# Performance work log

Measured on AMD Instinct MI355X. Metric: run time of the kernel, lower is better.

Reference implementation:

```python
import jax, jax.numpy as jnp
import numpy as np

B, XD, ZD, XE, H, NH = 8192, 4096, 1024, 64, 128, 4
NUM_STEPS, STEP, NOISE = 10, 0.01, 1.0
EPS = 1e-5


def setup_inputs() -> dict:
    key = jax.random.key(0)
    ks = jax.random.split(key, 16)
    w = lambda k, s: jax.random.normal(k, s, jnp.float32) * 0.02
    inp = {"x": jax.random.normal(ks[0], (B, XD), jnp.float32)}
    inp.update(
        px_W1=w(ks[1], (H, ZD)), px_b1=jnp.zeros(H, jnp.float32),
        px_W2=w(ks[2], (XD, H)), px_b2=jnp.zeros(XD, jnp.float32),
        emb_W=w(ks[3], (XE, XD)), emb_b=jnp.zeros(XE, jnp.float32),
        xp_W=w(ks[4], (H, XE)), xp_b=jnp.zeros(H, jnp.float32),
        zp_W=w(ks[5], (H, ZD)), zp_b=jnp.zeros(H, jnp.float32),
        sa_Wqkv=w(ks[6], (3 * H, H)), sa_bqkv=jnp.zeros(3 * H, jnp.float32),
        sa_Wo=w(ks[7], (H, H)), sa_bo=jnp.zeros(H, jnp.float32),
        ca_Wqkv=w(ks[8], (3 * H, H)), ca_bqkv=jnp.zeros(3 * H, jnp.float32),
        ca_Wo=w(ks[9], (H, H)), ca_bo=jnp.zeros(H, jnp.float32),
        ffn_W1=w(ks[10], (H, H)), ffn_b1=jnp.zeros(H, jnp.float32),
        ffn_W2=w(ks[11], (H, H)), ffn_b2=jnp.zeros(H, jnp.float32),
        ln1_g=jnp.ones(H, jnp.float32), ln1_b=jnp.zeros(H, jnp.float32),
        ln2_g=jnp.ones(H, jnp.float32), ln2_b=jnp.zeros(H, jnp.float32),
        ln3_g=jnp.ones(H, jnp.float32), ln3_b=jnp.zeros(H, jnp.float32),
        out_W=w(ks[12], (1, H)), out_b=jnp.zeros(1, jnp.float32),
    )
    return inp


def _ln(x, g, b):
    m = jnp.mean(x, -1, keepdims=True)
    v = jnp.var(x, -1, keepdims=True)
    return (x - m) * jax.lax.rsqrt(v + EPS) * g + b


def _mha(q, k, v, Wqkv, bqkv, Wo, bo):
    # torch nn.MultiheadAttention math, batch-first layout (B, S, E)
    E = q.shape[-1]
    d = E // NH
    Wq, Wk, Wv = jnp.split(Wqkv, 3, 0)
    bq, bk, bv = jnp.split(bqkv, 3, 0)
    hd = lambda t, W, bb: (t @ W.T + bb).reshape(t.shape[0], t.shape[1], NH, d)
    qh, kh, vh = hd(q, Wq, bq), hd(k, Wk, bk), hd(v, Wv, bv)
    s = jnp.einsum('bqhd,bkhd->bhqk', qh, kh) / jnp.sqrt(jnp.float32(d))
    a = jax.nn.softmax(s, -1)
    o = jnp.einsum('bhqk,bkhd->bqhd', a, vh).reshape(q.shape[0], q.shape[1], E)
    return o @ Wo.T + bo


def _forward(x, px_W1, px_b1, px_W2, px_b2, emb_W, emb_b, xp_W, xp_b, zp_W, zp_b,
             sa_Wqkv, sa_bqkv, sa_Wo, sa_bo, ca_Wqkv, ca_bqkv, ca_Wo, ca_bo,
             ffn_W1, ffn_b1, ffn_W2, ffn_b2, ln1_g, ln1_b, ln2_g, ln2_b,
             ln3_g, ln3_b, out_W, out_b):
    bsz = x.shape[0]
    px = lambda z: jax.nn.relu(z @ px_W1.T + px_b1) @ px_W2.T + px_b2
    grad_fn = jax.grad(lambda z: jnp.sum((px(z) - x) ** 2))
    ks = jax.random.split(jax.random.key(42), NUM_STEPS + 1)
    z0 = jax.random.normal(ks[0], (bsz, ZD), jnp.float32)

    def step(z, k):
        z = z - 0.5 * STEP * grad_fn(z)
        z = z + NOISE * jnp.sqrt(jnp.float32(STEP)) * jax.random.normal(k, z.shape, z.dtype)
        return z, None

    z, _ = jax.lax.scan(step, z0, ks[1:])
    z = jax.lax.stop_gradient(z)  # torch: z.detach()

    x_recon = px(z)                               # (B, XD)
    x_tok = (x @ emb_W.T + emb_b)[:, None, :]     # (B, 1, XE)
    z_lat = z[:, None, :]                         # (B, 1, ZD)
    x_h = x_tok @ xp_W.T + xp_b                   # (B, 1, H)
    z_h = z_lat @ zp_W.T + zp_b                   # (B, 1, H)
    sa = _mha(x_h, x_h, x_h, sa_Wqkv, sa_bqkv, sa_Wo, sa_bo)
    h1 = _ln(x_h + sa, ln1_g, ln1_b)
    ca = _mha(h1, z_h, z_h, ca_Wqkv, ca_bqkv, ca_Wo, ca_bo)
    h2 = _ln(h1 + ca, ln2_g, ln2_b)
    ff = jax.nn.relu(h2 @ ffn_W1.T + ffn_b1) @ ffn_W2.T + ffn_b2
    h3 = _ln(h2 + ff, ln3_g, ln3_b)
    y_pred = h3 @ out_W.T + out_b                 # (B, 1, 1)
    return x_recon, y_pred


def reference(x, px_W1, px_b1, px_W2, px_b2, emb_W, emb_b, xp_W, xp_b, zp_W, zp_b,
              sa_Wqkv, sa_bqkv, sa_Wo, sa_bo, ca_Wqkv, ca_bqkv, ca_Wo, ca_bo,
              ffn_W1, ffn_b1, ffn_W2, ffn_b2, ln1_g, ln1_b, ln2_g, ln2_b,
              ln3_g, ln3_b, out_W, out_b):
    return _forward(x, px_W1, px_b1, px_W2, px_b2, emb_W, emb_b, xp_W, xp_b,
                    zp_W, zp_b, sa_Wqkv, sa_bqkv, sa_Wo, sa_bo, ca_Wqkv,
                    ca_bqkv, ca_Wo, ca_bo, ffn_W1, ffn_b1, ffn_W2, ffn_b2,
                    ln1_g, ln1_b, ln2_g, ln2_b, ln3_g, ln3_b, out_W, out_b)
```

## Files before the change

### kernel.cpp

```cpp
#include <hip/hip_runtime.h>
#include <hip/hip_bf16.h>
#include <cstdint>
#include <cstddef>
#include <cmath>

#define B_     8192
#define XD_    4096
#define ZD_    1024
#define XE_    64
#define H_     128
#define ZN_    (B_*ZD_)

typedef __attribute__((ext_vector_type(8))) short short8_t;
typedef __attribute__((ext_vector_type(4))) float f32x4_t;
#define MFMA16(a,b,c) __builtin_amdgcn_mfma_f32_16x16x32_bf16((a),(b),(c),0,0,0)

__host__ __device__ __forceinline__ uint32_t rotl32_(uint32_t x, int r){
#ifdef __HIP_DEVICE_COMPILE__
  return __builtin_rotateleft32(x, (uint32_t)r);
#else
  return (x<<r)|(x>>(32-r));
#endif
}

__host__ __device__ __forceinline__ void tf2x32(uint32_t k0, uint32_t k1,
                                                uint32_t x0, uint32_t x1,
                                                uint32_t* o0, uint32_t* o1){
  uint32_t k2 = k0 ^ k1 ^ 0x1BD11BDAu;
  x0 += k0; x1 += k1;
  x0 += x1; x1 = rotl32_(x1,13); x1 ^= x0;
  x0 += x1; x1 = rotl32_(x1,15); x1 ^= x0;
  x0 += x1; x1 = rotl32_(x1,26); x1 ^= x0;
  x0 += x1; x1 = rotl32_(x1, 6); x1 ^= x0;
  x0 += k1; x1 += k2 + 1u;
  x0 += x1; x1 = rotl32_(x1,17); x1 ^= x0;
  x0 += x1; x1 = rotl32_(x1,29); x1 ^= x0;
  x0 += x1; x1 = rotl32_(x1,16); x1 ^= x0;
  x0 += x1; x1 = rotl32_(x1,24); x1 ^= x0;
  x0 += k2; x1 += k0 + 2u;
  x0 += x1; x1 = rotl32_(x1,13); x1 ^= x0;
  x0 += x1; x1 = rotl32_(x1,15); x1 ^= x0;
  x0 += x1; x1 = rotl32_(x1,26); x1 ^= x0;
  x0 += x1; x1 = rotl32_(x1, 6); x1 ^= x0;
  x0 += k0; x1 += k1 + 3u;
  x0 += x1; x1 = rotl32_(x1,17); x1 ^= x0;
  x0 += x1; x1 = rotl32_(x1,29); x1 ^= x0;
  x0 += x1; x1 = rotl32_(x1,16); x1 ^= x0;
  x0 += x1; x1 = rotl32_(x1,24); x1 ^= x0;
  x0 += k1; x1 += k2 + 4u;
  x0 += x1; x1 = rotl32_(x1,13); x1 ^= x0;
  x0 += x1; x1 = rotl32_(x1,15); x1 ^= x0;
  x0 += x1; x1 = rotl32_(x1,26); x1 ^= x0;
  x0 += x1; x1 = rotl32_(x1, 6); x1 ^= x0;
  x0 += k2; x1 += k0 + 5u;
  *o0 = x0; *o1 = x1;
}

__device__ __forceinline__ float erfinv_(float x){
  float w = -__logf(fmaf(-x, x, 1.0f));
  float p;
  if (w < 5.0f){
    w -= 2.5f;
    p = 2.81022636e-08f;
    p = fmaf(p, w, 3.43273939e-07f);
    p = fmaf(p, w, -3.5233877e-06f);
    p = fmaf(p, w, -4.39150654e-06f);
    p = fmaf(p, w, 0.00021858087f);
    p = fmaf(p, w, -0.00125372503f);
    p = fmaf(p, w, -0.00417768164f);
    p = fmaf(p, w, 0.246640727f);
    p = fmaf(p, w, 1.50140941f);
  } else {
    w = sqrtf(w) - 3.0f;
    p = -0.000200214257f;
    p = fmaf(p, w, 0.000100950558f);
    p = fmaf(p, w, 0.00134934322f);
    p = fmaf(p, w, -0.00367342844f);
    p = fmaf(p, w, 0.00573950773f);
    p = fmaf(p, w, -0.0076224613f);
    p = fmaf(p, w, 0.00943887047f);
    p = fmaf(p, w, 1.00167406f);
    p = fmaf(p, w, 2.83297682f);
  }
  return p * x;
}

__device__ __forceinline__ float bits_to_normal(uint32_t bits){
  float f = __uint_as_float((bits >> 9) | 0x3f800000u) - 1.0f;
  float u = fmaxf(-0.99999994f, fmaf(f, 2.0f, -0.99999994f));
  return 1.41421356f * erfinv_(u);
}

__device__ __forceinline__ float rng_normal(uint32_t k0, uint32_t k1, uint32_t idx){
  uint32_t o0, o1; tf2x32(k0, k1, 0u, idx, &o0, &o1);
  return bits_to_normal(o0 ^ o1);
}

__device__ __forceinline__ ushort f2bf(float f){
  return __builtin_bit_cast(ushort, __float2bfloat16(f));
}
__device__ __forceinline__ float bf2f(ushort u){ return __uint_as_float(((uint32_t)u) << 16); }

__device__ __forceinline__ void gen8(uint32_t k0, uint32_t k1, uint32_t base, uint4* g){
  union { ushort u[8]; uint4 q; } pk;
  #pragma unroll
  for (int j = 0; j < 8; ++j) pk.u[j] = f2bf(rng_normal(k0,k1,base+(uint32_t)j));
  *g = pk.q;
}

__global__ void k_prepAB(const float* __restrict__ saWo, const float* __restrict__ saWqkv,
                         const float* __restrict__ caWo, const float* __restrict__ caWqkv,
                         const float* __restrict__ sabqkv, const float* __restrict__ sabo,
                         const float* __restrict__ cabqkv, const float* __restrict__ cabo,
                         const float* __restrict__ W2, const float* __restrict__ pb2,
                         float* __restrict__ S, float* __restrict__ U,
                         float* __restrict__ s0, float* __restrict__ u0, float* __restrict__ cb,
                         uint32_t* __restrict__ dkeys){
  int blk = blockIdx.x, tid = threadIdx.x;
  if (blk < 512){
    int idx = (blk & 255) * 64 + tid;
    int i = idx >> 7, j = idx & 127;
    if (blk < 256){
      float acc = (i == j) ? 1.0f : 0.0f;
      for (int k = 0; k < H_; ++k) acc += saWo[i*H_ + k] * saWqkv[(2*H_ + k)*H_ + j];
      S[idx] = acc;
    } else {
      float acc = 0.0f;
      for (int k = 0; k < H_; ++k) acc += caWo[i*H_ + k] * caWqkv[(2*H_ + k)*H_ + j];
      U[idx] = acc;
    }
  } else {
    int b2 = blk - 512;
    if (b2 == 0 && tid == 0){
      for (uint32_t i = 0; i < 11; ++i){
        uint32_t a, b; tf2x32(0u, 42u, 0u, i, &a, &b);
        dkeys[2*i] = a; dkeys[2*i+1] = b;
      }
    }
    if (b2 < 2){
      int i = b2*64 + tid;
      float acc = sabo[i];
      for (int k = 0; k < H_; ++k) acc += saWo[i*H_ + k] * sabqkv[2*H_ + k];
      s0[i] = acc;
    } else if (b2 < 4){
      int i = (b2-2)*64 + tid;
      float acc = cabo[i];
      for (int k = 0; k < H_; ++k) acc += caWo[i*H_ + k] * cabqkv[2*H_ + k];
      u0[i] = acc;
    } else {
      int j = (b2-4)*64 + tid;
      float acc = 0.0f;
      for (int c = 0; c < XD_; ++c) acc += pb2[c] * W2[(size_t)c*H_ + j];
      cb[j] = acc;
    }
  }
}

__global__ void k_prepTR(const float* __restrict__ S, const float* __restrict__ U,
                         const float* __restrict__ xpW, const float* __restrict__ zpW,
                         const float* __restrict__ xpb, const float* __restrict__ zpb,
                         const float* __restrict__ s0, const float* __restrict__ u0,
                         float* __restrict__ T, float* __restrict__ R,
                         float* __restrict__ t0, float* __restrict__ r0v){
  int blk = blockIdx.x, tid = threadIdx.x;
  if (blk < 128){
    int idx = blk*64 + tid;
    int i = idx >> 6, e = idx & 63;
    float acc = 0.0f;
    for (int m = 0; m < H_; ++m) acc += S[i*H_ + m] * xpW[m*XE_ + e];
    T[idx] = acc;
  } else if (blk < 2176){
    int idx = (blk-128)*64 + tid;
    int i = idx >> 10, k = idx & 1023;
    float acc = 0.0f;
    for (int m = 0; m < H_; ++m) acc += U[i*H_ + m] * zpW[(size_t)m*ZD_ + k];
    R[idx] = acc;
  } else if (blk < 2178){
    int i = (blk-2176)*64 + tid;
    float acc = s0[i];
    for (int m = 0; m < H_; ++m) acc += S[i*H_ + m] * xpb[m];
    t0[i] = acc;
  } else {
    int i = (blk-2178)*64 + tid;
    float acc = u0[i];
    for (int m = 0; m < H_; ++m) acc += U[i*H_ + m] * zpb[m];
    r0v[i] = acc;
  }
}

__global__ void k_prepWM(const float* __restrict__ W2, const float* __restrict__ T,
                         const float* __restrict__ embW, const float* __restrict__ embb,
                         const float* __restrict__ t0, const float* __restrict__ W1,
                         const float* __restrict__ R,
                         ushort* __restrict__ WXT, float* __restrict__ q0,
                         float* __restrict__ Mpart, float* __restrict__ Gpart){
  if (blockIdx.x < 4096){
    int idx = blockIdx.x*256 + threadIdx.x;
    int j = idx >> 12, c = idx & 4095;
    float v;
    if (j < H_) v = W2[(size_t)c*H_ + j];
    else {
      int i = j - H_;
      float acc = 0.0f;
      for (int e = 0; e < XE_; ++e) acc += T[i*XE_ + e] * embW[(size_t)e*XD_ + c];
      v = acc;
    }
    WXT[idx] = f2bf(v);
    if (idx < H_){
      float acc = t0[idx];
      for (int e = 0; e < XE_; ++e) acc += T[idx*XE_ + e] * embb[e];
      q0[idx] = acc;
    }
  } else {
    int gid = (blockIdx.x - 4096)*256 + threadIdx.x;
    if (gid < 131072){
      int slice = gid >> 14, i = gid & 16383;
      int j1 = i >> 7, j2 = i & 127;
      int c0 = slice*512;
      float acc = 0.0f;
      for (int c = c0; c < c0+512; ++c)
        acc += W2[(size_t)c*H_ + j1] * W2[(size_t)c*H_ + j2];
      Mpart[(size_t)slice*16384 + i] = acc;
    } else {
      int g = gid - 131072;
      int slice = g >> 15, i2 = g & 32767;
      int i = i2 >> 7, k = i2 & 127;
      int m0 = slice*128;
      float acc = 0.0f;
      if (i < 128){
        for (int m = m0; m < m0+128; ++m)
          acc += W1[(size_t)i*ZD_ + m] * W1[(size_t)k*ZD_ + m];
      } else {
        for (int m = m0; m < m0+128; ++m)
          acc += W1[(size_t)k*ZD_ + m] * R[(size_t)(i-128)*ZD_ + m];
      }
      Gpart[(size_t)slice*32768 + i2] = acc;
    }
  }
}

__global__ void k_conv(const float* __restrict__ W2, const float* __restrict__ W1,
                       const float* __restrict__ R,
                       const float* __restrict__ Mpart, const float* __restrict__ Gpart,
                       ushort* __restrict__ W2bf, ushort* __restrict__ Mbf,
                       ushort* __restrict__ FBT, ushort* __restrict__ GGr){
  int idx = blockIdx.x*256 + threadIdx.x;
  if (idx < 524288) W2bf[idx] = f2bf(W2[idx]);
  else if (idx < 540672){
    int i = idx - 524288;
    float s = 0.0f;
    #pragma unroll
    for (int p = 0; p < 8; ++p) s += Mpart[(size_t)p*16384 + i];
    Mbf[i] = f2bf(2.0f*s);
  } else if (idx < 802816){
    int i = idx - 540672;
    int j    = i & 7;
    int lane = (i >> 3) & 63;
    int hh   = (i >> 9) & 1;
    int itt  = (i >> 10) & 15;
    int cf   = i >> 14;
    int srow = cf*16 + (lane & 15);
    int scol = itt*64 + hh*32 + ((lane >> 4) << 3) + j;
    float v = (srow < H_) ? W1[(size_t)srow*ZD_ + scol] : R[(size_t)(srow-H_)*ZD_ + scol];
    FBT[i] = f2bf(v);
  } else {
    int i = idx - 802816;
    float s = 0.0f;
    #pragma unroll
    for (int p = 0; p < 8; ++p) s += Gpart[(size_t)p*32768 + i];
    GGr[i] = f2bf(-0.005f*s);
  }
}

__global__ __launch_bounds__(256) void k_noiseproj(
    const ushort* __restrict__ FBT, const uint32_t* __restrict__ dkeys,
    float* __restrict__ y0c0, ushort* __restrict__ NWR){
  const int t = threadIdx.x, lane = t & 63, w = t >> 6;
  const int l15 = lane & 15, rq = (lane >> 4)*4, kq8 = (lane >> 4)*8;
  (void)kq8;
  const int gwid = blockIdx.x*4 + w;
  const int p = gwid >> 9, mb = gwid & 511;
  const int row0 = mb*16;
  const uint32_t k0 = dkeys[2*p], k1 = dkeys[2*p+1];
  const uint32_t rbase = (uint32_t)(row0 + l15)*1024u + (uint32_t)((lane >> 4)*8);
  f32x4_t acc[16] = {};
  #pragma unroll 1
  for (int it = 0; it < 16; ++it){
    uint4 br[16];
    {
      const ushort* fb = FBT + (size_t)(it*2)*512 + lane*8;
      #pragma unroll
      for (int cf = 0; cf < 16; ++cf) br[cf] = *(const uint4*)(fb + (size_t)cf*16384);
    }
    __builtin_amdgcn_sched_barrier(0);
    uint4 g0; gen8(k0, k1, rbase + (uint32_t)(it*64), &g0);
    short8_t a0 = __builtin_bit_cast(short8_t, g0);
    #pragma unroll
    for (int cf = 0; cf < 16; ++cf)
      acc[cf] = MFMA16(a0, __builtin_bit_cast(short8_t, br[cf]), acc[cf]);
    {
      const ushort* fb = FBT + (size_t)(it*2+1)*512 + lane*8;
      #pragma unroll
      for (int cf = 0; cf < 16; ++cf) br[cf] = *(const uint4*)(fb + (size_t)cf*16384);
    }
    __builtin_amdgcn_sched_barrier(0);
    uint4 g1; gen8(k0, k1, rbase + (uint32_t)(it*64 + 32), &g1);
    short8_t a1 = __builtin_bit_cast(short8_t, g1);
    #pragma unroll
    for (int cf = 0; cf < 16; ++cf)
      acc[cf] = MFMA16(a1, __builtin_bit_cast(short8_t, br[cf]), acc[cf]);
  }
  #pragma unroll
  for (int cf = 0; cf < 16; ++cf){
    int col = cf*16 + l15;
    #pragma unroll
    for (int r = 0; r < 4; ++r){
      int row = row0 + rq + r;
      float v = acc[cf][r];
      if (p == 0) y0c0[(size_t)row*256 + col] = v;
      else NWR[(size_t)(p-1)*2097152 + (size_t)row*256 + col] = f2bf(0.1f*v);
    }
  }
}

__global__ __launch_bounds__(256) void k_xpass_mfma(
    const float* __restrict__ x, const ushort* __restrict__ WXT,
    const float* __restrict__ cb, const float* __restrict__ q0,
    float* __restrict__ cneg, float* __restrict__ h1pre){
  __shared__ __align__(16) ushort xt[2][32*72];
  __shared__ __align__(16) ushort bt[2][128*72];
  const int t = threadIdx.x, lane = t & 63, w = t >> 6;
  const int bm = blockIdx.x >> 1, bn = blockIdx.x & 1;
  const int row0 = bm*32, ncol0 = bn*128;
  const int l15 = lane & 15, kq8 = (lane >> 4)*8, rq = (lane >> 4)*4;
  const int rt = w & 1, cb4 = (w >> 1)*4;
  const int xr = t >> 3, xk = (t & 7)*8;
  const int wn = t >> 1, wk = (t & 1)*32;
  f32x4_t acc[4] = {};
  {
    float4 v0 = *(const float4*)&x[(size_t)(row0+xr)*XD_ + xk];
    float4 v1 = *(const float4*)&x[(size_t)(row0+xr)*XD_ + xk + 4];
    union { ushort u[8]; uint4 q; } p;
    p.u[0]=f2bf(v0.x); p.u[1]=f2bf(v0.y); p.u[2]=f2bf(v0.z); p.u[3]=f2bf(v0.w);
    p.u[4]=f2bf(v1.x); p.u[5]=f2bf(v1.y); p.u[6]=f2bf(v1.z); p.u[7]=f2bf(v1.w);
    *(uint4*)&xt[0][xr*72 + xk] = p.q;
    const ushort* s = &WXT[(size_t)(ncol0+wn)*XD_ + wk];
    uint4 b0v=*(const uint4*)s, b1v=*(const uint4*)(s+8), b2v=*(const uint4*)(s+16), b3v=*(const uint4*)(s+24);
    ushort* d = &bt[0][wn*72 + wk];
    *(uint4*)d=b0v; *(uint4*)(d+8)=b1v; *(uint4*)(d+16)=b2v; *(uint4*)(d+24)=b3v;
  }
  float4 xv0, xv1; uint4 wb0, wb1, wb2, wb3;
  {
    xv0 = *(const float4*)&x[(size_t)(row0+xr)*XD_ + 64 + xk];
    xv1 = *(const float4*)&x[(size_t)(row0+xr)*XD_ + 64 + xk + 4];
    const ushort* s = &WXT[(size_t)(ncol0+wn)*XD_ + 64 + wk];
    wb0=*(const uint4*)s; wb1=*(const uint4*)(s+8); wb2=*(const uint4*)(s+16); wb3=*(const uint4*)(s+24);
  }
  #pragma unroll 1
  for (int it = 0; it < 64; ++it){
    __syncthreads();
    if (it < 63){
      union { ushort u[8]; uint4 q; } p;
      p.u[0]=f2bf(xv0.x); p.u[1]=f2bf(xv0.y); p.u[2]=f2bf(xv0.z); p.u[3]=f2bf(xv0.w);
      p.u[4]=f2bf(xv1.x); p.u[5]=f2bf(xv1.y); p.u[6]=f2bf(xv1.z); p.u[7]=f2bf(xv1.w);
      *(uint4*)&xt[(it+1)&1][xr*72 + xk] = p.q;
      ushort* d = &bt[(it+1)&1][wn*72 + wk];
      *(uint4*)d=wb0; *(uint4*)(d+8)=wb1; *(uint4*)(d+16)=wb2; *(uint4*)(d+24)=wb3;
    }
    if (it < 62){
      const int kt = (it+2)*64;
      xv0 = *(const float4*)&x[(size_t)(row0+xr)*XD_ + kt + xk];
      xv1 = *(const float4*)&x[(size_t)(row0+xr)*XD_ + kt + xk + 4];
      const ushort* s = &WXT[(size_t)(ncol0+wn)*XD_ + kt + wk];
      wb0=*(const uint4*)s; wb1=*(const uint4*)(s+8); wb2=*(const uint4*)(s+16); wb3=*(const uint4*)(s+24);
    }
    const ushort* xb = &xt[it&1][(rt*16+l15)*72];
    const ushort* bb = &bt[it&1][0];
    #pragma unroll
    for (int h = 0; h < 2; ++h){
      short8_t a = *(const short8_t*)(xb + h*32 + kq8);
      #pragma unroll
      for (int c = 0; c < 4; ++c){
        short8_t b = *(const short8_t*)(bb + ((cb4+c)*16+l15)*72 + h*32 + kq8);
        acc[c] = MFMA16(a, b, acc[c]);
      }
    }
  }
  #pragma unroll
  for (int c = 0; c < 4; ++c){
    int jl = (cb4+c)*16 + l15;
    #pragma unroll
    for (int r = 0; r < 4; ++r){
      int row = row0 + rt*16 + rq + r;
      float v = acc[c][r];
      if (bn == 0) cneg[(size_t)row*H_ + jl] = 2.0f*(cb[jl] - v);
      else         h1pre[(size_t)row*H_ + jl] = v + q0[jl];
    }
  }
}

__global__ __launch_bounds__(512) void k_lv2(
    const ushort* __restrict__ M2bf, const ushort* __restrict__ GGr,
    const float* __restrict__ y0c0, const ushort* __restrict__ NWR,
    const float* __restrict__ b1, const float* __restrict__ r0v,
    const float* __restrict__ cneg,
    ushort* __restrict__ hfin_bf, float* __restrict__ capre){
  __shared__ __align__(16) ushort abuf[16*136];
  __shared__ __align__(16) ushort glbuf[16*136];
  const int t = threadIdx.x, lane = t & 63, w = t >> 6;
  const int l15 = lane & 15, kq8 = (lane >> 4)*8, rq = (lane >> 4)*4;
  const int b0 = blockIdx.x * 16;
  const int myc = w*16 + l15;
  const int col2 = w*32 + l15;

  f32x4_t acc[2];
  #pragma unroll
  for (int nf = 0; nf < 2; ++nf)
    #pragma unroll
    for (int r = 0; r < 4; ++r)
      acc[nf][r] = y0c0[(size_t)(b0+rq+r)*256 + col2 + nf*16];
  float cn[4];
  #pragma unroll
  for (int r = 0; r < 4; ++r) cn[r] = cneg[(size_t)(b0+rq+r)*H_ + myc];
  float bb2[2];
  bb2[0] = (w < 4) ? b1[col2] : 0.0f;
  bb2[1] = (w < 4) ? b1[col2+16] : 0.0f;
  ushort nx[8];
  #pragma unroll
  for (int nf = 0; nf < 2; ++nf)
    #pragma unroll
    for (int r = 0; r < 4; ++r)
      nx[nf*4+r] = NWR[(size_t)(b0+rq+r)*256 + col2 + nf*16];

  #pragma unroll 1
  for (int s = 0; s < 10; ++s){
    if (w < 4){
      #pragma unroll
      for (int nf = 0; nf < 2; ++nf)
        #pragma unroll
        for (int r = 0; r < 4; ++r)
          abuf[(rq+r)*136 + col2 + nf*16] = f2bf(fmaxf(acc[nf][r] + bb2[nf], 0.0f));
    }
    __syncthreads();
    f32x4_t g2 = {};
    #pragma unroll
    for (int h = 0; h < 4; ++h){
      short8_t a = *(const short8_t*)&abuf[l15*136 + h*32 + kq8];
      short8_t b = *(const short8_t*)&M2bf[(size_t)myc*H_ + h*32 + kq8];
      g2 = MFMA16(a, b, g2);
    }
    #pragma unroll
    for (int r = 0; r < 4; ++r){
      float g = (abuf[(rq+r)*136 + myc] != 0) ? (g2[r] + cn[r]) : 0.0f;
      glbuf[(rq+r)*136 + myc] = f2bf(g);
    }
    __syncthreads();
    #pragma unroll
    for (int nf = 0; nf < 2; ++nf)
      #pragma unroll
      for (int h = 0; h < 4; ++h){
        short8_t a = *(const short8_t*)&glbuf[l15*136 + h*32 + kq8];
        short8_t b = *(const short8_t*)&GGr[(size_t)(col2 + nf*16)*H_ + h*32 + kq8];
        acc[nf] = MFMA16(a, b, acc[nf]);
      }
    #pragma unroll
    for (int nf = 0; nf < 2; ++nf)
      #pragma unroll
      for (int r = 0; r < 4; ++r)
        acc[nf][r] += bf2f(nx[nf*4+r]);
    if (s < 9){
      #pragma unroll
      for (int nf = 0; nf < 2; ++nf)
        #pragma unroll
        for (int r = 0; r < 4; ++r)
          nx[nf*4+r] = NWR[(size_t)(s+1)*2097152 + (size_t)(b0+rq+r)*256 + col2 + nf*16];
    }
    __syncthreads();
  }
  if (w < 4){
    #pragma unroll
    for (int nf = 0; nf < 2; ++nf)
      #pragma unroll
      for (int r = 0; r < 4; ++r)
        hfin_bf[(size_t)(b0+rq+r)*H_ + col2 + nf*16] = f2bf(fmaxf(acc[nf][r] + bb2[nf], 0.0f));
  } else {
    #pragma unroll
    for (int nf = 0; nf < 2; ++nf)
      #pragma unroll
      for (int r = 0; r < 4; ++r)
        capre[(size_t)(b0+rq+r)*H_ + (col2 + nf*16 - 128)] = acc[nf][r] + r0v[col2 + nf*16 - 128];
  }
}

__global__ __launch_bounds__(256) void k_xrecon_mfma(
    const ushort* __restrict__ hfin_bf, const ushort* __restrict__ W2bf,
    const float* __restrict__ b2, float* __restrict__ out){
  __shared__ __align__(16) ushort at[64*136];
  __shared__ __align__(16) ushort bt[128*136];
  const int tid = threadIdx.x, lane = tid & 63, w = tid >> 6;
  const int bm = blockIdx.x >> 5, bn = blockIdx.x & 31;
  const int row0 = bm*64, c0 = bn*128;
  const int l15 = lane & 15, kq8 = (lane >> 4)*8, rq = (lane >> 4)*4;
  { int r = tid >> 2, kq = (tid & 3)*32;
    const ushort* src = &hfin_bf[(size_t)(row0 + r)*H_ + kq];
    #pragma unroll
    for (int i = 0; i < 4; ++i) *(uint4*)&at[r*136 + kq + 8*i] = *(const uint4*)(src + 8*i);
  }
  { int n = tid >> 1, kh = (tid & 1)*64;
    const ushort* src = &W2bf[(size_t)(c0 + n)*H_ + kh];
    #pragma unroll
    for (int i = 0; i < 8; ++i) *(uint4*)&bt[n*136 + kh + 8*i] = *(const uint4*)(src + 8*i);
  }
  __syncthreads();
  f32x4_t acc[8] = {};
  #pragma unroll
  for (int k = 0; k < 4; ++k){
    short8_t a = *(const short8_t*)&at[(w*16 + l15)*136 + k*32 + kq8];
    #pragma unroll
    for (int nf = 0; nf < 8; ++nf){
      short8_t b = *(const short8_t*)&bt[(nf*16 + l15)*136 + k*32 + kq8];
      acc[nf] = MFMA16(a, b, acc[nf]);
    }
  }
  #pragma unroll
  for (int nf = 0; nf < 8; ++nf){
    int c = c0 + nf*16 + l15;
    float bbv = b2[c];
    #pragma unroll
    for (int r = 0; r < 4; ++r){
      int row = row0 + w*16 + rq + r;
      out[(size_t)row*XD_ + c] = acc[nf][r] + bbv;
    }
  }
}

__device__ __forceinline__ float wsum64(float v){
  #pragma unroll
  for (int off = 32; off > 0; off >>= 1) v += __shfl_xor(v, off, 64);
  return v;
}

__global__ __launch_bounds__(256) void k_tail(
    const float* __restrict__ h1pre, const float* __restrict__ capre,
    const float* __restrict__ ln1g, const float* __restrict__ ln1b,
    const float* __restrict__ ln2g, const float* __restrict__ ln2b,
    const float* __restrict__ ln3g, const float* __restrict__ ln3b,
    const float* __restrict__ fW1, const float* __restrict__ fb1,
    const float* __restrict__ fW2, const float* __restrict__ fb2,
    const float* __restrict__ outW, const float* __restrict__ outb,
    float* __restrict__ y){
  __shared__ float sh2[4][128];
  __shared__ float st1[4][128];
  const int tid = threadIdx.x;
  const int w = tid >> 6;
  const int l = tid & 63;
  const int b = blockIdx.x * 4 + w;
  const float* hp = h1pre + (size_t)b * H_;
  const float* cp = capre + (size_t)b * H_;
  float x0 = hp[l], x1 = hp[l+64];
  float m = wsum64(x0 + x1) * (1.0f/128.0f);
  float d0 = x0 - m, d1 = x1 - m;
  float v = wsum64(d0*d0 + d1*d1) * (1.0f/128.0f);
  float rs = rsqrtf(v + 1e-5f);
  float h1a = d0 * rs * ln1g[l]    + ln1b[l];
  float h1b = d1 * rs * ln1g[l+64] + ln1b[l+64];
  x0 = h1a + cp[l]; x1 = h1b + cp[l+64];
  m = wsum64(x0 + x1) * (1.0f/128.0f);
  d0 = x0 - m; d1 = x1 - m;
  v = wsum64(d0*d0 + d1*d1) * (1.0f/128.0f);
  rs = rsqrtf(v + 1e-5f);
  float h2a = d0 * rs * ln2g[l]    + ln2b[l];
  float h2b = d1 * rs * ln2g[l+64] + ln2b[l+64];
  sh2[w][l] = h2a; sh2[w][l+64] = h2b;
  __syncthreads();
  float ta = fb1[l], tb = fb1[l+64];
  #pragma unroll 8
  for (int m4 = 0; m4 < H_; m4 += 4){
    float4 hv = *(const float4*)&sh2[w][m4];
    float4 wa = *(const float4*)&fW1[(size_t)l*H_ + m4];
    float4 wb = *(const float4*)&fW1[(size_t)(l+64)*H_ + m4];
    ta = fmaf(wa.x, hv.x, ta); ta = fmaf(wa.y, hv.y, ta); ta = fmaf(wa.z, hv.z, ta); ta = fmaf(wa.w, hv.w, ta);
    tb = fmaf(wb.x, hv.x, tb); tb = fmaf(wb.y, hv.y, tb); tb = fmaf(wb.z, hv.z, tb); tb = fmaf(wb.w, hv.w, tb);
  }
  ta = fmaxf(ta, 0.0f); tb = fmaxf(tb, 0.0f);
  st1[w][l] = ta; st1[w][l+64] = tb;
  __syncthreads();
  float fa = fb2[l], fbv = fb2[l+64];
  #pragma unroll 8
  for (int m4 = 0; m4 < H_; m4 += 4){
    float4 tv = *(const float4*)&st1[w][m4];
    float4 wa = *(const float4*)&fW2[(size_t)l*H_ + m4];
    float4 wb = *(const float4*)&fW2[(size_t)(l+64)*H_ + m4];
    fa  = fmaf(wa.x, tv.x, fa);  fa  = fmaf(wa.y, tv.y, fa);  fa  = fmaf(wa.z, tv.z, fa);  fa  = fmaf(wa.w, tv.w, fa);
    fbv = fmaf(wb.x, tv.x, fbv); fbv = fmaf(wb.y, tv.y, fbv); fbv = fmaf(wb.z, tv.z, fbv); fbv = fmaf(wb.w, tv.w, fbv);
  }
  x0 = h2a + fa; x1 = h2b + fbv;
  m = wsum64(x0 + x1) * (1.0f/128.0f);
  d0 = x0 - m; d1 = x1 - m;
  v = wsum64(d0*d0 + d1*d1) * (1.0f/128.0f);
  rs = rsqrtf(v + 1e-5f);
  float h3a = d0 * rs * ln3g[l]    + ln3b[l];
  float h3b = d1 * rs * ln3g[l+64] + ln3b[l+64];
  float py = wsum64(outW[l]*h3a + outW[l+64]*h3b);
  if (l == 0) y[b] = py + outb[0];
}

extern "C" void kernel_launch(void* const* d_in, const int* in_sizes, int n_in,
                              void* d_out, int out_size, void* d_ws, size_t ws_size,
                              hipStream_t stream){
  const float* x      = (const float*)d_in[0];
  const float* pxW1   = (const float*)d_in[1];
  const float* pxb1   = (const float*)d_in[2];
  const float* pxW2   = (const float*)d_in[3];
  const float* pxb2   = (const float*)d_in[4];
  const float* embW   = (const float*)d_in[5];
  const float* embb   = (const float*)d_in[6];
  const float* xpW    = (const float*)d_in[7];
  const float* xpb    = (const float*)d_in[8];
  const float* zpW    = (const float*)d_in[9];
  const float* zpb    = (const float*)d_in[10];
  const float* saWqkv = (const float*)d_in[11];
  const float* sabqkv = (const float*)d_in[12];
  const float* saWo   = (const float*)d_in[13];
  const float* sabo   = (const float*)d_in[14];
  const float* caWqkv = (const float*)d_in[15];
  const float* cabqkv = (const float*)d_in[16];
  const float* caWo   = (const float*)d_in[17];
  const float* cabo   = (const float*)d_in[18];
  const float* fW1    = (const float*)d_in[19];
  const float* fb1    = (const float*)d_in[20];
  const float* fW2    = (const float*)d_in[21];
  const float* fb2    = (const float*)d_in[22];
  const float* ln1g   = (const float*)d_in[23];
  const float* ln1b   = (const float*)d_in[24];
  const float* ln2g   = (const float*)d_in[25];
  const float* ln2b   = (const float*)d_in[26];
  const float* ln3g   = (const float*)d_in[27];
  const float* ln3b   = (const float*)d_in[28];
  const float* outW   = (const float*)d_in[29];
  const float* outb   = (const float*)d_in[30];
  (void)in_sizes; (void)n_in; (void)out_size; (void)ws_size;

  float* ws    = (float*)d_ws;
  float* cneg  = ws;
  float* h1pre = cneg + (size_t)B_*H_;
  float* capre = h1pre + (size_t)B_*H_;
  float* Rm    = capre + (size_t)B_*H_;
  float* Sm    = Rm + (size_t)H_*ZD_;
  float* Um    = Sm + H_*H_;
  float* Tm    = Um + H_*H_;
  float* vs0   = Tm + H_*XE_;
  float* vu0   = vs0 + H_;
  float* vt0   = vu0 + H_;
  float* vq0   = vt0 + H_;
  float* vr0   = vq0 + H_;
  float* vcb   = vr0 + H_;
  float* Mpart = vcb + H_;
  float* Gpart = Mpart + 131072;
  uint32_t* dkeys = (uint32_t*)(Gpart + 262144);
  float* y0c0  = (float*)(dkeys + 32);
  ushort* WXT   = (ushort*)(y0c0 + (size_t)B_*256);
  ushort* W2bf  = WXT + (size_t)256*XD_;
  ushort* Mbf   = W2bf + (size_t)XD_*H_;
  ushort* FBT   = Mbf + H_*H_;
  ushort* GGr   = FBT + (size_t)256*ZD_;
  ushort* hfin  = GGr + (size_t)256*H_;
  ushort* NWR   = hfin + (size_t)B_*H_;

  float* xre   = (float*)d_out;
  float* ypred = xre + (size_t)B_*XD_;

  k_prepAB  <<<518,  64, 0, stream>>>(saWo, saWqkv, caWo, caWqkv, sabqkv, sabo,
                                      cabqkv, cabo, pxW2, pxb2, Sm, Um, vs0, vu0, vcb, dkeys);
  k_prepTR  <<<2180, 64, 0, stream>>>(Sm, Um, xpW, zpW, xpb, zpb, vs0, vu0, Tm, Rm, vt0, vr0);
  k_prepWM  <<<5632, 256, 0, stream>>>(pxW2, Tm, embW, embb, vt0, pxW1, Rm,
                                       WXT, vq0, Mpart, Gpart);
  k_conv    <<<3264, 256, 0, stream>>>(pxW2, pxW1, Rm, Mpart, Gpart, W2bf, Mbf, FBT, GGr);
  k_noiseproj <<<1408, 256, 0, stream>>>(FBT, dkeys, y0c0, NWR);
  k_xpass_mfma <<<512, 256, 0, stream>>>(x, WXT, vcb, vq0, cneg, h1pre);
  k_lv2     <<<512, 512, 0, stream>>>(Mbf, GGr, y0c0, NWR, pxb1, vr0, cneg, hfin, capre);
  k_xrecon_mfma <<<4096, 256, 0, stream>>>(hfin, W2bf, pxb2, xre);
  k_tail    <<<2048, 256, 0, stream>>>(h1pre, capre, ln1g, ln1b, ln2g, ln2b, ln3g, ln3b,
                                       fW1, fb1, fW2, fb2, outW, outb, ypred);
}
```

Measured before the change: 797.9 us.

## Merge noise projection with x-pass and fold tail into Langevin kernel

The noise-projection and x-pass GEMM kernels become one launch: blocks are interleaved 11:4 per group, so each group runs both kinds side by side and their work overlaps. The tail (layer norms, FFN, output head) now runs at the end of the Langevin kernel, reading cross-attention pre-activations from shared memory. This removes the capre global buffer and two launches. In exchange, the merged kernel carries the larger register and shared-memory footprint of both paths, which can lower occupancy, and the Langevin kernel gains serial tail work per block.

```diff
diff --git a/kernel.cpp b/kernel.cpp
--- a/kernel.cpp
+++ b/kernel.cpp
@@ -272,141 +272,159 @@
   }
 }
 
-__global__ __launch_bounds__(256) void k_noiseproj(
+__global__ __launch_bounds__(256) void k_npx2(
     const ushort* __restrict__ FBT, const uint32_t* __restrict__ dkeys,
-    float* __restrict__ y0c0, ushort* __restrict__ NWR){
+    float* __restrict__ y0c0, ushort* __restrict__ NWR,
+    const float* __restrict__ x, const ushort* __restrict__ WXT,
+    const float* __restrict__ cb, const float* __restrict__ q0v,
+    float* __restrict__ cneg, float* __restrict__ h1pre){
+  __shared__ __align__(16) ushort smem[23040];
   const int t = threadIdx.x, lane = t & 63, w = t >> 6;
   const int l15 = lane & 15, rq = (lane >> 4)*4, kq8 = (lane >> 4)*8;
-  (void)kq8;
-  const int gwid = blockIdx.x*4 + w;
-  const int p = gwid >> 9, mb = gwid & 511;
-  const int row0 = mb*16;
-  const uint32_t k0 = dkeys[2*p], k1 = dkeys[2*p+1];
-  const uint32_t rbase = (uint32_t)(row0 + l15)*1024u + (uint32_t)((lane >> 4)*8);
-  f32x4_t acc[16] = {};
-  #pragma unroll 1
-  for (int it = 0; it < 16; ++it){
-    uint4 br[16];
+  const int grp = blockIdx.x / 15, rem = blockIdx.x % 15;
+
+  if (rem < 11){
+    const int gwid = (grp*11 + rem)*4 + w;
+    const int p = gwid >> 9, mb = gwid & 511;
+    const int row0 = mb*16;
+    const uint32_t k0 = dkeys[2*p], k1 = dkeys[2*p+1];
+    const uint32_t rbase = (uint32_t)(row0 + l15)*1024u + (uint32_t)((lane >> 4)*8);
+    f32x4_t acc[16] = {};
+    #pragma unroll 1
+    for (int it = 0; it < 16; ++it){
+      uint4 br[16];
+      {
+        const ushort* fb = FBT + (size_t)(it*2)*512 + lane*8;
+        #pragma unroll
+        for (int cf = 0; cf < 16; ++cf) br[cf] = *(const uint4*)(fb + (size_t)cf*16384);
+      }
+      __builtin_amdgcn_sched_barrier(0);
+      uint4 g0; gen8(k0, k1, rbase + (uint32_t)(it*64), &g0);
+      short8_t a0 = __builtin_bit_cast(short8_t, g0);
+      #pragma unroll
+      for (int cf = 0; cf < 16; ++cf)
+        acc[cf] = MFMA16(a0, __builtin_bit_cast(short8_t, br[cf]), acc[cf]);
+      {
+        const ushort* fb = FBT + (size_t)(it*2+1)*512 + lane*8;
+        #pragma unroll
+        for (int cf = 0; cf < 16; ++cf) br[cf] = *(const uint4*)(fb + (size_t)cf*16384);
+      }
+      __builtin_amdgcn_sched_barrier(0);
+      uint4 g1; gen8(k0, k1, rbase + (uint32_t)(it*64 + 32), &g1);
+      short8_t a1 = __builtin_bit_cast(short8_t, g1);
+      #pragma unroll
+      for (int cf = 0; cf < 16; ++cf)
+        acc[cf] = MFMA16(a1, __builtin_bit_cast(short8_t, br[cf]), acc[cf]);
+    }
+    #pragma unroll
+    for (int cf = 0; cf < 16; ++cf){
+      int col = cf*16 + l15;
+      #pragma unroll
+      for (int r = 0; r < 4; ++r){
+        int row = row0 + rq + r;
+        float v = acc[cf][r];
+        if (p == 0) y0c0[(size_t)row*256 + col] = v;
+        else NWR[(size_t)(p-1)*2097152 + (size_t)row*256 + col] = f2bf(0.1f*v);
+      }
+    }
+  } else {
+    ushort* xt0 = smem;
+    ushort* xt1 = smem + 2304;
+    ushort* bt0 = smem + 4608;
+    ushort* bt1 = smem + 13824;
+    const int xp = grp*4 + (rem - 11);
+    const int bm = xp >> 1, bn = xp & 1;
+    const int row0 = bm*32, ncol0 = bn*128;
+    const int rt = w & 1, cb4 = (w >> 1)*4;
+    const int xr = t >> 3, xk = (t & 7)*8;
+    const int wn = t >> 1, wk = (t & 1)*32;
+    f32x4_t acc[4] = {};
     {
-      const ushort* fb = FBT + (size_t)(it*2)*512 + lane*8;
-      #pragma unroll
-      for (int cf = 0; cf < 16; ++cf) br[cf] = *(const uint4*)(fb + (size_t)cf*16384);
-    }
-    __builtin_amdgcn_sched_barrier(0);
-    uint4 g0; gen8(k0, k1, rbase + (uint32_t)(it*64), &g0);
-    short8_t a0 = __builtin_bit_cast(short8_t, g0);
-    #pragma unroll
-    for (int cf = 0; cf < 16; ++cf)
-      acc[cf] = MFMA16(a0, __builtin_bit_cast(short8_t, br[cf]), acc[cf]);
+      float4 v0 = *(const float4*)&x[(size_t)(row0+xr)*XD_ + xk];
+      float4 v1 = *(const float4*)&x[(size_t)(row0+xr)*XD_ + xk + 4];
+      union { ushort u[8]; uint4 q; } p;
+      p.u[0]=f2bf(v0.x); p.u[1]=f2bf(v0.y); p.u[2]=f2bf(v0.z); p.u[3]=f2bf(v0.w);
+      p.u[4]=f2bf(v1.x); p.u[5]=f2bf(v1.y); p.u[6]=f2bf(v1.z); p.u[7]=f2bf(v1.w);
+      *(uint4*)&xt0[xr*72 + xk] = p.q;
+      const ushort* s = &WXT[(size_t)(ncol0+wn)*XD_ + wk];
+      uint4 b0v=*(const uint4*)s, b1v=*(const uint4*)(s+8), b2v=*(const uint4*)(s+16), b3v=*(const uint4*)(s+24);
+      ushort* d = &bt0[wn*72 + wk];
+      *(uint4*)d=b0v; *(uint4*)(d+8)=b1v; *(uint4*)(d+16)=b2v; *(uint4*)(d+24)=b3v;
+    }
+    float4 xv0, xv1; uint4 wb0, wb1, wb2, wb3;
     {
-      const ushort* fb = FBT + (size_t)(it*2+1)*512 + lane*8;
-      #pragma unroll
-      for (int cf = 0; cf < 16; ++cf) br[cf] = *(const uint4*)(fb + (size_t)cf*16384);
-    }
-    __builtin_amdgcn_sched_barrier(0);
-    uint4 g1; gen8(k0, k1, rbase + (uint32_t)(it*64 + 32), &g1);
-    short8_t a1 = __builtin_bit_cast(short8_t, g1);
-    #pragma unroll
-    for (int cf = 0; cf < 16; ++cf)
-      acc[cf] = MFMA16(a1, __builtin_bit_cast(short8_t, br[cf]), acc[cf]);
-  }
+      xv0 = *(const float4*)&x[(size_t)(row0+xr)*XD_ + 64 + xk];
+      xv1 = *(const float4*)&x[(size_t)(row0+xr)*XD_ + 64 + xk + 4];
+      const ushort* s = &WXT[(size_t)(ncol0+wn)*XD_ + 64 + wk];
+      wb0=*(const uint4*)s; wb1=*(const uint4*)(s+8); wb2=*(const uint4*)(s+16); wb3=*(const uint4*)(s+24);
+    }
+    #pragma unroll 1
+    for (int it = 0; it < 64; ++it){
+      __syncthreads();
+      if (it < 63){
+        union { ushort u[8]; uint4 q; } p;
+        p.u[0]=f2bf(xv0.x); p.u[1]=f2bf(xv0.y); p.u[2]=f2bf(xv0.z); p.u[3]=f2bf(xv0.w);
+        p.u[4]=f2bf(xv1.x); p.u[5]=f2bf(xv1.y); p.u[6]=f2bf(xv1.z); p.u[7]=f2bf(xv1.w);
+        *(uint4*)&(((it+1)&1) ? xt1 : xt0)[xr*72 + xk] = p.q;
+        ushort* d = &(((it+1)&1) ? bt1 : bt0)[wn*72 + wk];
+        *(uint4*)d=wb0; *(uint4*)(d+8)=wb1; *(uint4*)(d+16)=wb2; *(uint4*)(d+24)=wb3;
+      }
+      if (it < 62){
+        const int kt = (it+2)*64;
+        xv0 = *(const float4*)&x[(size_t)(row0+xr)*XD_ + kt + xk];
+        xv1 = *(const float4*)&x[(size_t)(row0+xr)*XD_ + kt + xk + 4];
+        const ushort* s = &WXT[(size_t)(ncol0+wn)*XD_ + kt + wk];
+        wb0=*(const uint4*)s; wb1=*(const uint4*)(s+8); wb2=*(const uint4*)(s+16); wb3=*(const uint4*)(s+24);
+      }
+      const ushort* xb = &((it&1) ? xt1 : xt0)[(rt*16+l15)*72];
+      const ushort* bb = (it&1) ? bt1 : bt0;
+      #pragma unroll
+      for (int h = 0; h < 2; ++h){
+        short8_t a = *(const short8_t*)(xb + h*32 + kq8);
+        #pragma unroll
+        for (int c = 0; c < 4; ++c){
+          short8_t b = *(const short8_t*)(bb + ((cb4+c)*16+l15)*72 + h*32 + kq8);
+          acc[c] = MFMA16(a, b, acc[c]);
+        }
+      }
+    }
+    #pragma unroll
+    for (int c = 0; c < 4; ++c){
+      int jl = (cb4+c)*16 + l15;
+      #pragma unroll
+      for (int r = 0; r < 4; ++r){
+        int row = row0 + rt*16 + rq + r;
+        float v = acc[c][r];
+        if (bn == 0) cneg[(size_t)row*H_ + jl] = 2.0f*(cb[jl] - v);
+        else         h1pre[(size_t)row*H_ + jl] = v + q0v[jl];
+      }
+    }
+  }
+}
+
+__device__ __forceinline__ float wsum64(float v){
   #pragma unroll
-  for (int cf = 0; cf < 16; ++cf){
-    int col = cf*16 + l15;
-    #pragma unroll
-    for (int r = 0; r < 4; ++r){
-      int row = row0 + rq + r;
-      float v = acc[cf][r];
-      if (p == 0) y0c0[(size_t)row*256 + col] = v;
-      else NWR[(size_t)(p-1)*2097152 + (size_t)row*256 + col] = f2bf(0.1f*v);
-    }
-  }
-}
-
-__global__ __launch_bounds__(256) void k_xpass_mfma(
-    const float* __restrict__ x, const ushort* __restrict__ WXT,
-    const float* __restrict__ cb, const float* __restrict__ q0,
-    float* __restrict__ cneg, float* __restrict__ h1pre){
-  __shared__ __align__(16) ushort xt[2][32*72];
-  __shared__ __align__(16) ushort bt[2][128*72];
-  const int t = threadIdx.x, lane = t & 63, w = t >> 6;
-  const int bm = blockIdx.x >> 1, bn = blockIdx.x & 1;
-  const int row0 = bm*32, ncol0 = bn*128;
-  const int l15 = lane & 15, kq8 = (lane >> 4)*8, rq = (lane >> 4)*4;
-  const int rt = w & 1, cb4 = (w >> 1)*4;
-  const int xr = t >> 3, xk = (t & 7)*8;
-  const int wn = t >> 1, wk = (t & 1)*32;
-  f32x4_t acc[4] = {};
-  {
-    float4 v0 = *(const float4*)&x[(size_t)(row0+xr)*XD_ + xk];
-    float4 v1 = *(const float4*)&x[(size_t)(row0+xr)*XD_ + xk + 4];
-    union { ushort u[8]; uint4 q; } p;
-    p.u[0]=f2bf(v0.x); p.u[1]=f2bf(v0.y); p.u[2]=f2bf(v0.z); p.u[3]=f2bf(v0.w);
-    p.u[4]=f2bf(v1.x); p.u[5]=f2bf(v1.y); p.u[6]=f2bf(v1.z); p.u[7]=f2bf(v1.w);
-    *(uint4*)&xt[0][xr*72 + xk] = p.q;
-    const ushort* s = &WXT[(size_t)(ncol0+wn)*XD_ + wk];
-    uint4 b0v=*(const uint4*)s, b1v=*(const uint4*)(s+8), b2v=*(const uint4*)(s+16), b3v=*(const uint4*)(s+24);
-    ushort* d = &bt[0][wn*72 + wk];
-    *(uint4*)d=b0v; *(uint4*)(d+8)=b1v; *(uint4*)(d+16)=b2v; *(uint4*)(d+24)=b3v;
-  }
-  float4 xv0, xv1; uint4 wb0, wb1, wb2, wb3;
-  {
-    xv0 = *(const float4*)&x[(size_t)(row0+xr)*XD_ + 64 + xk];
-    xv1 = *(const float4*)&x[(size_t)(row0+xr)*XD_ + 64 + xk + 4];
-    const ushort* s = &WXT[(size_t)(ncol0+wn)*XD_ + 64 + wk];
-    wb0=*(const uint4*)s; wb1=*(const uint4*)(s+8); wb2=*(const uint4*)(s+16); wb3=*(const uint4*)(s+24);
-  }
-  #pragma unroll 1
-  for (int it = 0; it < 64; ++it){
-    __syncthreads();
-    if (it < 63){
-      union { ushort u[8]; uint4 q; } p;
-      p.u[0]=f2bf(xv0.x); p.u[1]=f2bf(xv0.y); p.u[2]=f2bf(xv0.z); p.u[3]=f2bf(xv0.w);
-      p.u[4]=f2bf(xv1.x); p.u[5]=f2bf(xv1.y); p.u[6]=f2bf(xv1.z); p.u[7]=f2bf(xv1.w);
-      *(uint4*)&xt[(it+1)&1][xr*72 + xk] = p.q;
-      ushort* d = &bt[(it+1)&1][wn*72 + wk];
-      *(uint4*)d=wb0; *(uint4*)(d+8)=wb1; *(uint4*)(d+16)=wb2; *(uint4*)(d+24)=wb3;
-    }
-    if (it < 62){
-      const int kt = (it+2)*64;
-      xv0 = *(const float4*)&x[(size_t)(row0+xr)*XD_ + kt + xk];
-      xv1 = *(const float4*)&x[(size_t)(row0+xr)*XD_ + kt + xk + 4];
-      const ushort* s = &WXT[(size_t)(ncol0+wn)*XD_ + kt + wk];
-      wb0=*(const uint4*)s; wb1=*(const uint4*)(s+8); wb2=*(const uint4*)(s+16); wb3=*(const uint4*)(s+24);
-    }
-    const ushort* xb = &xt[it&1][(rt*16+l15)*72];
-    const ushort* bb = &bt[it&1][0];
-    #pragma unroll
-    for (int h = 0; h < 2; ++h){
-      short8_t a = *(const short8_t*)(xb + h*32 + kq8);
-      #pragma unroll
-      for (int c = 0; c < 4; ++c){
-        short8_t b = *(const short8_t*)(bb + ((cb4+c)*16+l15)*72 + h*32 + kq8);
-        acc[c] = MFMA16(a, b, acc[c]);
-      }
-    }
-  }
-  #pragma unroll
-  for (int c = 0; c < 4; ++c){
-    int jl = (cb4+c)*16 + l15;
-    #pragma unroll
-    for (int r = 0; r < 4; ++r){
-      int row = row0 + rt*16 + rq + r;
-      float v = acc[c][r];
-      if (bn == 0) cneg[(size_t)row*H_ + jl] = 2.0f*(cb[jl] - v);
-      else         h1pre[(size_t)row*H_ + jl] = v + q0[jl];
-    }
-  }
-}
-
-__global__ __launch_bounds__(512) void k_lv2(
+  for (int off = 32; off > 0; off >>= 1) v += __shfl_xor(v, off, 64);
+  return v;
+}
+
+__global__ __launch_bounds__(512) void k_lv2t(
     const ushort* __restrict__ M2bf, const ushort* __restrict__ GGr,
     const float* __restrict__ y0c0, const ushort* __restrict__ NWR,
     const float* __restrict__ b1, const float* __restrict__ r0v,
-    const float* __restrict__ cneg,
-    ushort* __restrict__ hfin_bf, float* __restrict__ capre){
+    const float* __restrict__ cneg, const float* __restrict__ h1pre,
+    const float* __restrict__ ln1g, const float* __restrict__ ln1b,
+    const float* __restrict__ ln2g, const float* __restrict__ ln2b,
+    const float* __restrict__ ln3g, const float* __restrict__ ln3b,
+    const float* __restrict__ fW1, const float* __restrict__ fb1,
+    const float* __restrict__ fW2, const float* __restrict__ fb2,
+    const float* __restrict__ outW, const float* __restrict__ outb,
+    ushort* __restrict__ hfin_bf, float* __restrict__ ypred){
   __shared__ __align__(16) ushort abuf[16*136];
   __shared__ __align__(16) ushort glbuf[16*136];
+  __shared__ __align__(16) float caplds[16][132];
+  __shared__ __align__(16) float rowA[8][132];
+  __shared__ __align__(16) float rowB[8][132];
   const int t = threadIdx.x, lane = t & 63, w = t >> 6;
   const int l15 = lane & 15, kq8 = (lane >> 4)*8, rq = (lane >> 4)*4;
   const int b0 = blockIdx.x * 16;
@@ -488,7 +506,60 @@
     for (int nf = 0; nf < 2; ++nf)
       #pragma unroll
       for (int r = 0; r < 4; ++r)
-        capre[(size_t)(b0+rq+r)*H_ + (col2 + nf*16 - 128)] = acc[nf][r] + r0v[col2 + nf*16 - 128];
+        caplds[rq+r][col2 + nf*16 - 128] = acc[nf][r] + r0v[col2 + nf*16 - 128];
+  }
+  __syncthreads();
+
+  const int l = lane;
+  #pragma unroll 1
+  for (int j = 0; j < 2; ++j){
+    const int rloc = w*2 + j;
+    const int rr = b0 + rloc;
+    const float* hp = h1pre + (size_t)rr * H_;
+    float x0 = hp[l], x1 = hp[l+64];
+    float m = wsum64(x0 + x1) * (1.0f/128.0f);
+    float d0 = x0 - m, d1 = x1 - m;
+    float v = wsum64(d0*d0 + d1*d1) * (1.0f/128.0f);
+    float rs = rsqrtf(v + 1e-5f);
+    float h1a = d0 * rs * ln1g[l]    + ln1b[l];
+    float h1b = d1 * rs * ln1g[l+64] + ln1b[l+64];
+    x0 = h1a + caplds[rloc][l]; x1 = h1b + caplds[rloc][l+64];
+    m = wsum64(x0 + x1) * (1.0f/128.0f);
+    d0 = x0 - m; d1 = x1 - m;
+    v = wsum64(d0*d0 + d1*d1) * (1.0f/128.0f);
+    rs = rsqrtf(v + 1e-5f);
+    float h2a = d0 * rs * ln2g[l]    + ln2b[l];
+    float h2b = d1 * rs * ln2g[l+64] + ln2b[l+64];
+    rowA[w][l] = h2a; rowA[w][l+64] = h2b;
+    float ta = fb1[l], tb = fb1[l+64];
+    #pragma unroll 8
+    for (int m4 = 0; m4 < H_; m4 += 4){
+      float4 hv = *(const float4*)&rowA[w][m4];
+      float4 wa = *(const float4*)&fW1[(size_t)l*H_ + m4];
+      float4 wb = *(const float4*)&fW1[(size_t)(l+64)*H_ + m4];
+      ta = fmaf(wa.x, hv.x, ta); ta = fmaf(wa.y, hv.y, ta); ta = fmaf(wa.z, hv.z, ta); ta = fmaf(wa.w, hv.w, ta);
+      tb = fmaf(wb.x, hv.x, tb); tb = fmaf(wb.y, hv.y, tb); tb = fmaf(wb.z, hv.z, tb); tb = fmaf(wb.w, hv.w, tb);
+    }
+    ta = fmaxf(ta, 0.0f); tb = fmaxf(tb, 0.0f);
+    rowB[w][l] = ta; rowB[w][l+64] = tb;
+    float fa = fb2[l], fbv = fb2[l+64];
+    #pragma unroll 8
+    for (int m4 = 0; m4 < H_; m4 += 4){
+      float4 tv = *(const float4*)&rowB[w][m4];
+      float4 wa = *(const float4*)&fW2[(size_t)l*H_ + m4];
+      float4 wb = *(const float4*)&fW2[(size_t)(l+64)*H_ + m4];
+      fa  = fmaf(wa.x, tv.x, fa);  fa  = fmaf(wa.y, tv.y, fa);  fa  = fmaf(wa.z, tv.z, fa);  fa  = fmaf(wa.w, tv.w, fa);
+      fbv = fmaf(wb.x, tv.x, fbv); fbv = fmaf(wb.y, tv.y, fbv); fbv = fmaf(wb.z, tv.z, fbv); fbv = fmaf(wb.w, tv.w, fbv);
+    }
+    x0 = h2a + fa; x1 = h2b + fbv;
+    m = wsum64(x0 + x1) * (1.0f/128.0f);
+    d0 = x0 - m; d1 = x1 - m;
+    v = wsum64(d0*d0 + d1*d1) * (1.0f/128.0f);
+    rs = rsqrtf(v + 1e-5f);
+    float h3a = d0 * rs * ln3g[l]    + ln3b[l];
+    float h3b = d1 * rs * ln3g[l+64] + ln3b[l+64];
+    float py = wsum64(outW[l]*h3a + outW[l+64]*h3b);
+    if (l == 0) ypred[rr] = py + outb[0];
   }
 }
 
@@ -532,77 +603,6 @@
       out[(size_t)row*XD_ + c] = acc[nf][r] + bbv;
     }
   }
-}
-
-__device__ __forceinline__ float wsum64(float v){
-  #pragma unroll
-  for (int off = 32; off > 0; off >>= 1) v += __shfl_xor(v, off, 64);
-  return v;
-}
-
-__global__ __launch_bounds__(256) void k_tail(
-    const float* __restrict__ h1pre, const float* __restrict__ capre,
-    const float* __restrict__ ln1g, const float* __restrict__ ln1b,
-    const float* __restrict__ ln2g, const float* __restrict__ ln2b,
-    const float* __restrict__ ln3g, const float* __restrict__ ln3b,
-    const float* __restrict__ fW1, const float* __restrict__ fb1,
-    const float* __restrict__ fW2, const float* __restrict__ fb2,
-    const float* __restrict__ outW, const float* __restrict__ outb,
-    float* __restrict__ y){
-  __shared__ float sh2[4][128];
-  __shared__ float st1[4][128];
-  const int tid = threadIdx.x;
-  const int w = tid >> 6;
-  const int l = tid & 63;
-  const int b = blockIdx.x * 4 + w;
-  const float* hp = h1pre + (size_t)b * H_;
-  const float* cp = capre + (size_t)b * H_;
-  float x0 = hp[l], x1 = hp[l+64];
-  float m = wsum64(x0 + x1) * (1.0f/128.0f);
-  float d0 = x0 - m, d1 = x1 - m;
-  float v = wsum64(d0*d0 + d1*d1) * (1.0f/128.0f);
-  float rs = rsqrtf(v + 1e-5f);
-  float h1a = d0 * rs * ln1g[l]    + ln1b[l];
-  float h1b = d1 * rs * ln1g[l+64] + ln1b[l+64];
-  x0 = h1a + cp[l]; x1 = h1b + cp[l+64];
-  m = wsum64(x0 + x1) * (1.0f/128.0f);
-  d0 = x0 - m; d1 = x1 - m;
-  v = wsum64(d0*d0 + d1*d1) * (1.0f/128.0f);
-  rs = rsqrtf(v + 1e-5f);
-  float h2a = d0 * rs * ln2g[l]    + ln2b[l];
-  float h2b = d1 * rs * ln2g[l+64] + ln2b[l+64];
-  sh2[w][l] = h2a; sh2[w][l+64] = h2b;
-  __syncthreads();
-  float ta = fb1[l], tb = fb1[l+64];
-  #pragma unroll 8
-  for (int m4 = 0; m4 < H_; m4 += 4){
-    float4 hv = *(const float4*)&sh2[w][m4];
-    float4 wa = *(const float4*)&fW1[(size_t)l*H_ + m4];
-    float4 wb = *(const float4*)&fW1[(size_t)(l+64)*H_ + m4];
-    ta = fmaf(wa.x, hv.x, ta); ta = fmaf(wa.y, hv.y, ta); ta = fmaf(wa.z, hv.z, ta); ta = fmaf(wa.w, hv.w, ta);
-    tb = fmaf(wb.x, hv.x, tb); tb = fmaf(wb.y, hv.y, tb); tb = fmaf(wb.z, hv.z, tb); tb = fmaf(wb.w, hv.w, tb);
-  }
-  ta = fmaxf(ta, 0.0f); tb = fmaxf(tb, 0.0f);
-  st1[w][l] = ta; st1[w][l+64] = tb;
-  __syncthreads();
-  float fa = fb2[l], fbv = fb2[l+64];
-  #pragma unroll 8
-  for (int m4 = 0; m4 < H_; m4 += 4){
-    float4 tv = *(const float4*)&st1[w][m4];
-    float4 wa = *(const float4*)&fW2[(size_t)l*H_ + m4];
-    float4 wb = *(const float4*)&fW2[(size_t)(l+64)*H_ + m4];
-    fa  = fmaf(wa.x, tv.x, fa);  fa  = fmaf(wa.y, tv.y, fa);  fa  = fmaf(wa.z, tv.z, fa);  fa  = fmaf(wa.w, tv.w, fa);
-    fbv = fmaf(wb.x, tv.x, fbv); fbv = fmaf(wb.y, tv.y, fbv); fbv = fmaf(wb.z, tv.z, fbv); fbv = fmaf(wb.w, tv.w, fbv);
-  }
-  x0 = h2a + fa; x1 = h2b + fbv;
-  m = wsum64(x0 + x1) * (1.0f/128.0f);
-  d0 = x0 - m; d1 = x1 - m;
-  v = wsum64(d0*d0 + d1*d1) * (1.0f/128.0f);
-  rs = rsqrtf(v + 1e-5f);
-  float h3a = d0 * rs * ln3g[l]    + ln3b[l];
-  float h3b = d1 * rs * ln3g[l+64] + ln3b[l+64];
-  float py = wsum64(outW[l]*h3a + outW[l+64]*h3b);
-  if (l == 0) y[b] = py + outb[0];
 }
 
 extern "C" void kernel_launch(void* const* d_in, const int* in_sizes, int n_in,
@@ -644,8 +644,7 @@
   float* ws    = (float*)d_ws;
   float* cneg  = ws;
   float* h1pre = cneg + (size_t)B_*H_;
-  float* capre = h1pre + (size_t)B_*H_;
-  float* Rm    = capre + (size_t)B_*H_;
+  float* Rm    = h1pre + (size_t)B_*H_;
   float* Sm    = Rm + (size_t)H_*ZD_;
   float* Um    = Sm + H_*H_;
   float* Tm    = Um + H_*H_;
@@ -676,10 +675,9 @@
   k_prepWM  <<<5632, 256, 0, stream>>>(pxW2, Tm, embW, embb, vt0, pxW1, Rm,
                                        WXT, vq0, Mpart, Gpart);
   k_conv    <<<3264, 256, 0, stream>>>(pxW2, pxW1, Rm, Mpart, Gpart, W2bf, Mbf, FBT, GGr);
-  k_noiseproj <<<1408, 256, 0, stream>>>(FBT, dkeys, y0c0, NWR);
-  k_xpass_mfma <<<512, 256, 0, stream>>>(x, WXT, vcb, vq0, cneg, h1pre);
-  k_lv2     <<<512, 512, 0, stream>>>(Mbf, GGr, y0c0, NWR, pxb1, vr0, cneg, hfin, capre);
+  k_npx2    <<<1920, 256, 0, stream>>>(FBT, dkeys, y0c0, NWR, x, WXT, vcb, vq0, cneg, h1pre);
+  k_lv2t    <<<512, 512, 0, stream>>>(Mbf, GGr, y0c0, NWR, pxb1, vr0, cneg, h1pre,
+                                      ln1g, ln1b, ln2g, ln2b, ln3g, ln3b,
+                                      fW1, fb1, fW2, fb2, outW, outb, hfin, ypred);
   k_xrecon_mfma <<<4096, 256, 0, stream>>>(hfin, W2bf, pxb2, xre);
-  k_tail    <<<2048, 256, 0, stream>>>(h1pre, capre, ln1g, ln1b, ln2g, ln2b, ln3g, ln3b,
-                                       fW1, fb1, fW2, fb2, outW, outb, ypred);
-}
+}
```

After: 779.9 us. -2.2%, faster.
